# Kernel tuning notes

Measured on AMD Instinct MI355X. Metric: run time of the kernel, lower is better.

The kernel has to match this reference:

```python
import jax, jax.numpy as jnp
import numpy as np

B, T, S, C, E, H = 4, 2048, 2048, 256, 512, 8
D = E // H
SCALE = E ** (-0.5)


def setup_inputs() -> dict:
    key = jax.random.key(0)
    ks = jax.random.split(key, 12)
    x = jax.random.normal(ks[0], (B, T, C), dtype=jnp.float32)
    context = jax.random.normal(ks[1], (B, S, E), dtype=jnp.float32)
    pad_mask = jax.random.randint(ks[2], (B, T, S), 0, 2) == 1
    p = 0.02
    # Conv1d kernel_size=1 weights stored squeezed: [out_ch, in_ch]
    w_in = jax.random.normal(ks[3], (E, C), dtype=jnp.float32) * p
    b_in = jnp.zeros((E,), dtype=jnp.float32)
    wq = jax.random.normal(ks[4], (E, E), dtype=jnp.float32) * p
    bq = jnp.zeros((E,), dtype=jnp.float32)
    wk = jax.random.normal(ks[5], (E, E), dtype=jnp.float32) * p
    bk = jnp.zeros((E,), dtype=jnp.float32)
    wv = jax.random.normal(ks[6], (E, E), dtype=jnp.float32) * p
    bv = jnp.zeros((E,), dtype=jnp.float32)
    w_out = jax.random.normal(ks[7], (C, E), dtype=jnp.float32) * p
    b_out = jnp.zeros((C,), dtype=jnp.float32)
    return {"x": x, "context": context, "pad_mask": pad_mask,
            "w_in": w_in, "b_in": b_in, "wq": wq, "bq": bq,
            "wk": wk, "bk": bk, "wv": wv, "bv": bv,
            "w_out": w_out, "b_out": b_out}


def reference(x, context, pad_mask, w_in, b_in, wq, bq, wk, bk, wv, bv, w_out, b_out):
    # proj_in: Conv1d k=1 == per-token linear on channel dim. [B,T,C] -> [B,T,E]
    xe = jnp.einsum('btc,ec->bte', x, w_in) + b_in
    Q = (xe @ wq.T + bq).reshape(B, T, H, D)       # query tokens
    K = (context @ wk.T + bk).reshape(B, S, H, D)  # key tokens
    V = (context @ wv.T + bv).reshape(B, S, H, D)
    att = jnp.einsum('bihd,bjhd->bhij', Q, K) * SCALE  # [B,H,T,S]
    att = jnp.where(pad_mask[:, None, :, :], jnp.float32(-1e9), att)
    att = jax.nn.softmax(att, axis=-1)
    out = jnp.einsum('bhij,bjhd->bihd', att, V).reshape(B, T, E)
    # proj_out: Conv1d k=1, [B,T,E] -> [B,T,C]
    out = jnp.einsum('bte,ce->btc', out, w_out) + b_out
    return out
```

## Files before the change

### kernel.cpp

```cpp
#include <hip/hip_runtime.h>
#include <cstdint>
#include <cstddef>

#define Bb 4
#define Tt 2048
#define Ssz 2048
#define Cc 256
#define Ee 512
#define Hh 8

typedef short bf8 __attribute__((ext_vector_type(8)));
typedef float f4 __attribute__((ext_vector_type(4)));
typedef float f16v __attribute__((ext_vector_type(16)));
typedef unsigned int u32x2 __attribute__((ext_vector_type(2)));
typedef unsigned int u32x4 __attribute__((ext_vector_type(4)));

__device__ __forceinline__ unsigned short f2bf(float x) {
  unsigned int u = __float_as_uint(x);
  u += 0x7fffu + ((u >> 16) & 1u);
  return (unsigned short)(u >> 16);
}

__device__ __forceinline__ bf8 cvt8(float4 a, float4 b) {
  bf8 r;
  r[0] = (short)f2bf(a.x); r[1] = (short)f2bf(a.y);
  r[2] = (short)f2bf(a.z); r[3] = (short)f2bf(a.w);
  r[4] = (short)f2bf(b.x); r[5] = (short)f2bf(b.y);
  r[6] = (short)f2bf(b.z); r[7] = (short)f2bf(b.w);
  return r;
}

#if __has_builtin(__builtin_amdgcn_perm)
#define PACK2(u0, u1) __builtin_amdgcn_perm((u1), (u0), 0x07060302u)
#else
#define PACK2(u0, u1) (((u0) >> 16) | ((u1) & 0xffff0000u))
#endif

#define EXPU(v) __float_as_uint(__builtin_amdgcn_exp2f(v))
#define MFMA32(a, b, c) __builtin_amdgcn_mfma_f32_32x32x16_bf16((a), (b), (c), 0, 0, 0)

__device__ __forceinline__ void pl32swap(unsigned int& a, unsigned int& b) {
#if __has_builtin(__builtin_amdgcn_permlane32_swap)
  u32x2 r = __builtin_amdgcn_permlane32_swap(a, b, false, false);
  a = r[0];
  b = r[1];
#else
  unsigned int ax = (unsigned int)__shfl_xor((int)a, 32);
  unsigned int bx = (unsigned int)__shfl_xor((int)b, 32);
  bool hi = (threadIdx.x & 32) != 0;
  unsigned int an = hi ? bx : a;
  unsigned int bn = hi ? b : ax;
  a = an;
  b = bn;
#endif
}

__global__ __launch_bounds__(256) void prep(const float* __restrict__ w_in,
                                            const float* __restrict__ b_in,
                                            const float* __restrict__ wq,
                                            const float* __restrict__ bq,
                                            const float* __restrict__ wk,
                                            const float* __restrict__ wv,
                                            const float* __restrict__ wo,
                                            unsigned short* __restrict__ wkvb,
                                            unsigned short* __restrict__ wob,
                                            unsigned short* __restrict__ wqin,
                                            float* __restrict__ bqinb, float qsc) {
  __shared__ unsigned short sh[128][72];
  const int bid = blockIdx.x, tid = threadIdx.x;
  if (bid < 512) {
    int i = bid * 256 + tid;
    const float* s = (i < 65536) ? wk : wv;
    int off = (i < 65536) ? i : i - 65536;
    float4 v = ((const float4*)s)[off];
    ushort4 o;
    o.x = f2bf(v.x); o.y = f2bf(v.y); o.z = f2bf(v.z); o.w = f2bf(v.w);
    ((ushort4*)wkvb)[i] = o;
  } else if (bid < 640) {
    int i = (bid - 512) * 256 + tid;
    float4 v = ((const float4*)wo)[i];
    ushort4 o;
    o.x = f2bf(v.x); o.y = f2bf(v.y); o.z = f2bf(v.z); o.w = f2bf(v.w);
    ((ushort4*)wob)[i] = o;
  } else if (bid < 672) {
    const int idx = bid - 640;
    const int m0 = (idx & 7) * 64, n0 = (idx >> 3) * 64;
    unsigned short (*As)[72] = (unsigned short (*)[72]) & sh[0][0];
    unsigned short (*Bs)[72] = (unsigned short (*)[72]) & sh[64][0];
    const int wave = tid >> 6, lane = tid & 63;
    const int lrow = lane & 15, quad = lane >> 4;
    const int wm = (wave >> 1) * 32, wn = (wave & 1) * 32;
    const int arow = tid >> 3, ac = tid & 7;
    f4 acc[2][2];
#pragma unroll
    for (int i = 0; i < 2; i++)
#pragma unroll
      for (int j = 0; j < 2; j++) {
        f4 z = {0.f, 0.f, 0.f, 0.f};
        acc[i][j] = z;
      }
    for (int kt = 0; kt < 8; kt++) {
#pragma unroll
      for (int i = 0; i < 2; i++) {
        int row = arow + i * 32;
        const float* src = wq + (size_t)(m0 + row) * Ee + kt * 64 + ac * 8;
        float4 v0 = *(const float4*)src, v1 = *(const float4*)(src + 4);
        bf8 av;
        av[0] = (short)f2bf(v0.x * qsc); av[1] = (short)f2bf(v0.y * qsc);
        av[2] = (short)f2bf(v0.z * qsc); av[3] = (short)f2bf(v0.w * qsc);
        av[4] = (short)f2bf(v1.x * qsc); av[5] = (short)f2bf(v1.y * qsc);
        av[6] = (short)f2bf(v1.z * qsc); av[7] = (short)f2bf(v1.w * qsc);
        *(bf8*)&As[row][ac * 8] = av;
        int c = n0 + row;
        bf8 bv;
#pragma unroll
        for (int k = 0; k < 8; k++)
          bv[k] = (short)f2bf(w_in[(size_t)(kt * 64 + ac * 8 + k) * Cc + c]);
        *(bf8*)&Bs[row][ac * 8] = bv;
      }
      __syncthreads();
#pragma unroll
      for (int kk = 0; kk < 2; kk++) {
        bf8 af[2], bff[2];
#pragma unroll
        for (int i = 0; i < 2; i++) af[i] = *(const bf8*)&As[wm + i * 16 + lrow][kk * 32 + quad * 8];
#pragma unroll
        for (int j = 0; j < 2; j++) bff[j] = *(const bf8*)&Bs[wn + j * 16 + lrow][kk * 32 + quad * 8];
#pragma unroll
        for (int i = 0; i < 2; i++)
#pragma unroll
          for (int j = 0; j < 2; j++)
            acc[i][j] = __builtin_amdgcn_mfma_f32_16x16x32_bf16(af[i], bff[j], acc[i][j], 0, 0, 0);
      }
      __syncthreads();
    }
#pragma unroll
    for (int j = 0; j < 2; j++)
#pragma unroll
      for (int i = 0; i < 2; i++)
#pragma unroll
        for (int r = 0; r < 4; r++)
          wqin[(size_t)(m0 + wm + i * 16 + quad * 4 + r) * Cc + n0 + wn + j * 16 + lrow] =
              f2bf(acc[i][j][r]);
  } else {
    const int o = (bid - 672) * 32 + (tid >> 3);
    const int k0 = (tid & 7) * 64;
    float s = 0.f;
#pragma unroll
    for (int i = 0; i < 16; i++) {
      float4 w = *(const float4*)(wq + (size_t)o * Ee + k0 + i * 4);
      float4 bb = *(const float4*)(b_in + k0 + i * 4);
      s += w.x * bb.x + w.y * bb.y + w.z * bb.z + w.w * bb.w;
    }
    s += __shfl_xor(s, 1);
    s += __shfl_xor(s, 2);
    s += __shfl_xor(s, 4);
    if ((tid & 7) == 0) bqinb[o] = (s + bq[o]) * qsc;
  }
}

__global__ __launch_bounds__(256) void qkv(const float* __restrict__ x,
                                           const float* __restrict__ ctx,
                                           const unsigned short* __restrict__ wqin,
                                           const float* __restrict__ bqinb,
                                           const unsigned short* __restrict__ wkv,
                                           const float* __restrict__ bk,
                                           const float* __restrict__ bv,
                                           unsigned short* __restrict__ Qb,
                                           unsigned short* __restrict__ Kb,
                                           unsigned short* __restrict__ Vt,
                                           const int* __restrict__ mask,
                                           unsigned int* __restrict__ mp) {
  __shared__ unsigned short As[128][72];
  __shared__ unsigned short Bs[128][72];
  const int bid = blockIdx.x, tid = threadIdx.x;
  if (bid >= 768) {
    int i = (bid - 768) * 256 + tid;
    const int4* src = (const int4*)mask + (size_t)i * 8;
    unsigned int w = 0;
#pragma unroll
    for (int k = 0; k < 8; k++) {
      int4 v = src[k];
      w |= (unsigned int)(v.x != 0) << (k * 4);
      w |= (unsigned int)(v.y != 0) << (k * 4 + 1);
      w |= (unsigned int)(v.z != 0) << (k * 4 + 2);
      w |= (unsigned int)(v.w != 0) << (k * 4 + 3);
    }
    mp[i] = w;
    return;
  }
  const bool isQ = bid < 256;
  const int idx = isQ ? bid : bid - 256;
  const int m0 = (idx & 63) * 128;
  const int n0 = (idx >> 6) * 128;
  const int K = isQ ? 256 : 512;
  const float* A = isQ ? x : ctx;
  const unsigned short* Bt = isQ ? wqin : wkv;

  const int wave = tid >> 6, lane = tid & 63;
  const int lrow = lane & 15, quad = lane >> 4;
  const int wm = (wave >> 1) * 64, wn = (wave & 1) * 64;
  const int arow = tid >> 3, ac = tid & 7;

  f4 acc[4][4];
#pragma unroll
  for (int i = 0; i < 4; i++)
#pragma unroll
    for (int j = 0; j < 4; j++) {
      f4 z = {0.f, 0.f, 0.f, 0.f};
      acc[i][j] = z;
    }

  float4 ap0[4], ap1[4];
  bf8 bpre[4];
#pragma unroll
  for (int i = 0; i < 4; i++) {
    const float* src = A + (size_t)(m0 + arow + i * 32) * K + ac * 8;
    ap0[i] = *(const float4*)src;
    ap1[i] = *(const float4*)(src + 4);
    bpre[i] = *(const bf8*)(Bt + (size_t)(n0 + arow + i * 32) * K + ac * 8);
  }

  const int nkt = K >> 6;
  for (int kt = 0; kt < nkt; ++kt) {
#pragma unroll
    for (int i = 0; i < 4; i++) {
      *(bf8*)&As[arow + i * 32][ac * 8] = cvt8(ap0[i], ap1[i]);
      *(bf8*)&Bs[arow + i * 32][ac * 8] = bpre[i];
    }
    __syncthreads();
    if (kt + 1 < nkt) {
      int k0 = (kt + 1) << 6;
#pragma unroll
      for (int i = 0; i < 4; i++) {
        const float* src = A + (size_t)(m0 + arow + i * 32) * K + k0 + ac * 8;
        ap0[i] = *(const float4*)src;
        ap1[i] = *(const float4*)(src + 4);
        bpre[i] = *(const bf8*)(Bt + (size_t)(n0 + arow + i * 32) * K + k0 + ac * 8);
      }
    }
#pragma unroll
    for (int kk = 0; kk < 2; kk++) {
      bf8 af[4], bff[4];
#pragma unroll
      for (int i = 0; i < 4; i++)
        af[i] = *(const bf8*)&As[wm + i * 16 + lrow][kk * 32 + quad * 8];
#pragma unroll
      for (int j = 0; j < 4; j++)
        bff[j] = *(const bf8*)&Bs[wn + j * 16 + lrow][kk * 32 + quad * 8];
#pragma unroll
      for (int i = 0; i < 4; i++)
#pragma unroll
        for (int j = 0; j < 4; j++)
          acc[i][j] = __builtin_amdgcn_mfma_f32_16x16x32_bf16(af[i], bff[j],
                                                              acc[i][j], 0, 0, 0);
    }
    __syncthreads();
  }

  if (isQ) {
#pragma unroll
    for (int j = 0; j < 4; j++) {
      int col = n0 + wn + j * 16 + lrow;
      float bvv = bqinb[col];
#pragma unroll
      for (int i = 0; i < 4; i++)
#pragma unroll
        for (int r = 0; r < 4; r++)
          Qb[(size_t)(m0 + wm + i * 16 + quad * 4 + r) * Ee + col] =
              f2bf(acc[i][j][r] + bvv);
    }
  } else if (n0 < 512) {
#pragma unroll
    for (int j = 0; j < 4; j++) {
      int col = n0 + wn + j * 16 + lrow;
      float bvv = bk[col];
#pragma unroll
      for (int i = 0; i < 4; i++)
#pragma unroll
        for (int r = 0; r < 4; r++)
          Kb[(size_t)(m0 + wm + i * 16 + quad * 4 + r) * Ee + col] =
              f2bf(acc[i][j][r] + bvv);
    }
  } else {
#pragma unroll
    for (int j = 0; j < 4; j++) {
      int d = n0 - 512 + wn + j * 16 + lrow;
      int h = d >> 6, dd = d & 63;
      float bvv = bv[d];
#pragma unroll
      for (int i = 0; i < 4; i++) {
        int tok = m0 + wm + i * 16 + quad * 4;
        int b = tok >> 11, sl = tok & 2047;
        ushort4 pk;
        pk.x = f2bf(acc[i][j][0] + bvv);
        pk.y = f2bf(acc[i][j][1] + bvv);
        pk.z = f2bf(acc[i][j][2] + bvv);
        pk.w = f2bf(acc[i][j][3] + bvv);
        *(ushort4*)(Vt + (size_t)((b * Hh + h) * 64 + dd) * Ssz + sl) = pk;
      }
    }
  }
}

template <bool OUT_BF16, int BM, int BN, int WGM>
__global__ __launch_bounds__(256) void gemm_bt(const unsigned short* __restrict__ A,
                                               const unsigned short* __restrict__ Bt,
                                               const float* __restrict__ bias0,
                                               void* __restrict__ Cout,
                                               int M, int N, int K) {
  constexpr int WGN = 4 / WGM;
  constexpr int MI = BM / (WGM * 16);
  constexpr int NJ = BN / (WGN * 16);
  constexpr int NA = BM / 32;
  constexpr int NB = BN / 32;
  __shared__ unsigned short As[BM][72];
  __shared__ unsigned short Bs[BN][72];
  const int tid = threadIdx.x;
  const int wave = tid >> 6, lane = tid & 63;
  const int lrow = lane & 15, quad = lane >> 4;
  const int wm = (wave / WGN) * (BM / WGM);
  const int wn = (wave % WGN) * (BN / WGN);
  const int m0 = blockIdx.x * BM, n0 = blockIdx.y * BN;
  const int arow = tid >> 3, ac = tid & 7;

  f4 acc[MI][NJ];
#pragma unroll
  for (int i = 0; i < MI; i++)
#pragma unroll
    for (int j = 0; j < NJ; j++) {
      f4 z = {0.f, 0.f, 0.f, 0.f};
      acc[i][j] = z;
    }

  bf8 apre[NA], bpre[NB];
#pragma unroll
  for (int i = 0; i < NA; i++)
    apre[i] = *(const bf8*)(A + (size_t)(m0 + arow + i * 32) * K + ac * 8);
#pragma unroll
  for (int i = 0; i < NB; i++)
    bpre[i] = *(const bf8*)(Bt + (size_t)(n0 + arow + i * 32) * K + ac * 8);

  const int nkt = K >> 6;
  for (int kt = 0; kt < nkt; ++kt) {
#pragma unroll
    for (int i = 0; i < NA; i++) *(bf8*)&As[arow + i * 32][ac * 8] = apre[i];
#pragma unroll
    for (int i = 0; i < NB; i++) *(bf8*)&Bs[arow + i * 32][ac * 8] = bpre[i];
    __syncthreads();
    if (kt + 1 < nkt) {
      int k0 = (kt + 1) << 6;
#pragma unroll
      for (int i = 0; i < NA; i++)
        apre[i] = *(const bf8*)(A + (size_t)(m0 + arow + i * 32) * K + k0 + ac * 8);
#pragma unroll
      for (int i = 0; i < NB; i++)
        bpre[i] = *(const bf8*)(Bt + (size_t)(n0 + arow + i * 32) * K + k0 + ac * 8);
    }
#pragma unroll
    for (int kk = 0; kk < 2; kk++) {
      bf8 af[MI], bff[NJ];
#pragma unroll
      for (int i = 0; i < MI; i++)
        af[i] = *(const bf8*)&As[wm + i * 16 + lrow][kk * 32 + quad * 8];
#pragma unroll
      for (int j = 0; j < NJ; j++)
        bff[j] = *(const bf8*)&Bs[wn + j * 16 + lrow][kk * 32 + quad * 8];
#pragma unroll
      for (int i = 0; i < MI; i++)
#pragma unroll
        for (int j = 0; j < NJ; j++)
          acc[i][j] = __builtin_amdgcn_mfma_f32_16x16x32_bf16(af[i], bff[j],
                                                              acc[i][j], 0, 0, 0);
    }
    __syncthreads();
  }

#pragma unroll
  for (int j = 0; j < NJ; j++) {
    int col = n0 + wn + j * 16 + lrow;
    float bvv = bias0 ? bias0[col] : 0.f;
#pragma unroll
    for (int i = 0; i < MI; i++) {
#pragma unroll
      for (int r = 0; r < 4; r++) {
        int row = m0 + wm + i * 16 + quad * 4 + r;
        float v = acc[i][j][r] + bvv;
        if (OUT_BF16)
          ((unsigned short*)Cout)[(size_t)row * N + col] = f2bf(v);
        else
          ((float*)Cout)[(size_t)row * N + col] = v;
      }
    }
  }
}

__global__ __launch_bounds__(256, 2) void attn(const unsigned short* __restrict__ Q,
                                               const unsigned short* __restrict__ K,
                                               const unsigned short* __restrict__ Vt,
                                               const unsigned int* __restrict__ mp,
                                               unsigned short* __restrict__ O) {
  __shared__ unsigned short Ks[2][64][72];
  __shared__ unsigned short Vts[2][64][72];
  const int tid = threadIdx.x;
  const int wave = tid >> 6, lane = tid & 63;
  const int l31 = lane & 31, hi = lane >> 5;
  const int bid = blockIdx.x;
  const int bh = bid & 31, b = bh >> 3, h = bh & 7;
  const int t0 = (bid >> 5) * 128;
  const int wm = wave * 32;
  const int arow = tid >> 3, ac = tid & 7;

  const unsigned short* Qrow =
      Q + (size_t)(b * Tt + t0 + wm + l31) * Ee + h * 64 + hi * 8;
  bf8 qf[4];
#pragma unroll
  for (int c = 0; c < 4; c++) qf[c] = *(const bf8*)(Qrow + c * 16);

  f16v oacc0, oacc1, dacc;
#pragma unroll
  for (int r = 0; r < 16; r++) {
    oacc0[r] = 0.f;
    oacc1[r] = 0.f;
    dacc[r] = 0.f;
  }
  bf8 ones;
#pragma unroll
  for (int k = 0; k < 8; k++) ones[k] = (short)0x3F80;

  const unsigned short* Kbase = K + (size_t)b * Ssz * Ee + h * 64;
  const unsigned short* Vbase = Vt + (size_t)((b * Hh + h) * 64) * Ssz;
  const unsigned int* mroww = mp + (size_t)(b * Tt + t0 + wm + l31) * 64;

  bf8 kreg[2], vreg[2];
#pragma unroll
  for (int i = 0; i < 2; i++) {
    int row = arow + i * 32;
    kreg[i] = *(const bf8*)(Kbase + (size_t)row * Ee + ac * 8);
    vreg[i] = *(const bf8*)(Vbase + (size_t)row * Ssz + ac * 8);
  }
#pragma unroll
  for (int i = 0; i < 2; i++) {
    int row = arow + i * 32;
    *(bf8*)&Ks[0][row][ac * 8] = kreg[i];
    *(bf8*)&Vts[0][row][ac * 8] = vreg[i];
  }
  __syncthreads();

  for (int n = 0; n < 32; n++) {
    const int s0 = n * 64;
    const int cur = n & 1;
    if (n + 1 < 32) {
#pragma unroll
      for (int i = 0; i < 2; i++) {
        int row = arow + i * 32;
        kreg[i] = *(const bf8*)(Kbase + (size_t)(s0 + 64 + row) * Ee + ac * 8);
        vreg[i] = *(const bf8*)(Vbase + (size_t)row * Ssz + s0 + 64 + ac * 8);
      }
    }
    const uint2 mw = *(const uint2*)(mroww + (s0 >> 5));
    const unsigned int wsh0 = mw.x >> (4 * hi);
    const unsigned int wsh1 = mw.y >> (4 * hi);

    f16v sa0, sa1;
#pragma unroll
    for (int r = 0; r < 16; r++) {
      const int sh = (r & 3) + 8 * (r >> 2);
      sa0[r] = ((wsh0 >> sh) & 1u) ? -1e9f : 0.f;
      sa1[r] = ((wsh1 >> sh) & 1u) ? -1e9f : 0.f;
    }
#pragma unroll
    for (int c = 0; c < 4; c++) {
      bf8 kf0 = *(const bf8*)&Ks[cur][l31][c * 16 + hi * 8];
      bf8 kf1 = *(const bf8*)&Ks[cur][32 + l31][c * 16 + hi * 8];
      sa0 = MFMA32(kf0, qf[c], sa0);
      sa1 = MFMA32(kf1, qf[c], sa1);
    }
    unsigned int X0[8], X1[8];
#pragma unroll
    for (int m = 0; m < 8; m++) {
      X0[m] = PACK2(EXPU(sa0[2 * m]), EXPU(sa0[2 * m + 1]));
      X1[m] = PACK2(EXPU(sa1[2 * m]), EXPU(sa1[2 * m + 1]));
    }
#pragma unroll
    for (int c = 0; c < 4; c++) {
      const int m0 = 4 * (c & 1);
      unsigned int a0, a1, a2, a3;
      if (c < 2) {
        a0 = X0[m0]; a1 = X0[m0 + 1]; a2 = X0[m0 + 2]; a3 = X0[m0 + 3];
      } else {
        a0 = X1[m0]; a1 = X1[m0 + 1]; a2 = X1[m0 + 2]; a3 = X1[m0 + 3];
      }
      pl32swap(a0, a2);
      pl32swap(a1, a3);
      u32x4 pdv;
      pdv[0] = a0; pdv[1] = a1; pdv[2] = a2; pdv[3] = a3;
      bf8 pa = *(bf8*)&pdv;
      bf8 vf0 = *(const bf8*)&Vts[cur][l31][c * 16 + hi * 8];
      bf8 vf1 = *(const bf8*)&Vts[cur][32 + l31][c * 16 + hi * 8];
      dacc = MFMA32(pa, ones, dacc);
      oacc0 = MFMA32(pa, vf0, oacc0);
      oacc1 = MFMA32(pa, vf1, oacc1);
    }
    if (n + 1 < 32) {
#pragma unroll
      for (int i = 0; i < 2; i++) {
        int row = arow + i * 32;
        *(bf8*)&Ks[cur ^ 1][row][ac * 8] = kreg[i];
        *(bf8*)&Vts[cur ^ 1][row][ac * 8] = vreg[i];
      }
    }
    __syncthreads();
  }

#pragma unroll
  for (int r = 0; r < 16; r++) {
    const int tl = (r & 3) + 8 * (r >> 2) + 4 * hi;
    const float inv = 1.0f / dacc[r];
    const size_t off = (size_t)(b * Tt + t0 + wm + tl) * Ee + h * 64 + l31;
    O[off] = f2bf(oacc0[r] * inv);
    O[off + 32] = f2bf(oacc1[r] * inv);
  }
}

extern "C" void kernel_launch(void* const* d_in, const int* in_sizes, int n_in,
                              void* d_out, int out_size, void* d_ws, size_t ws_size,
                              hipStream_t stream) {
  const float* x    = (const float*)d_in[0];
  const float* ctx  = (const float*)d_in[1];
  const int*   mask = (const int*)d_in[2];
  const float* w_in = (const float*)d_in[3];
  const float* b_in = (const float*)d_in[4];
  const float* wq   = (const float*)d_in[5];
  const float* bq   = (const float*)d_in[6];
  const float* wk   = (const float*)d_in[7];
  const float* bk   = (const float*)d_in[8];
  const float* wv   = (const float*)d_in[9];
  const float* bv   = (const float*)d_in[10];
  const float* wo   = (const float*)d_in[11];
  const float* bo   = (const float*)d_in[12];

  const float qsc = 0.04419417382415922f * 1.4426950408889634f;

  unsigned short* ws = (unsigned short*)d_ws;
  unsigned int*   maskp = (unsigned int*)ws;
  unsigned short* wkvb  = ws + 1048576;
  unsigned short* wob   = ws + 1572864;
  unsigned short* wqin  = ws + 1703936;
  float*          bqinb = (float*)(ws + 1835008);
  unsigned short* Qb    = ws + 1836032;
  unsigned short* Kb    = ws + 6030336;
  unsigned short* Vtb   = ws + 10224640;
  unsigned short* Ob    = ws + 14418944;

  prep<<<688, 256, 0, stream>>>(w_in, b_in, wq, bq, wk, wv, wo,
                                wkvb, wob, wqin, bqinb, qsc);
  qkv<<<2816, 256, 0, stream>>>(x, ctx, wqin, bqinb, wkvb, bk, bv, Qb, Kb, Vtb,
                                mask, maskp);
  attn<<<512, 256, 0, stream>>>(Qb, Kb, Vtb, maskp, Ob);
  gemm_bt<false, 64, 64, 2><<<dim3(128, 4), 256, 0, stream>>>(
      Ob, wob, bo, d_out, 8192, 256, 512);
}
```

Measured before the change: 228.3 us.

## Process 64 query rows per wave in attention to reuse K/V fragments

Each attention wave now handles two 32-row query blocks instead of one, so each K and V fragment read from shared memory feeds twice as many MFMAs. The block tile grows to 256 query rows, the grid halves to 256 blocks, and launch bounds drop to one block per SM to make room for the doubled accumulators. This cuts LDS traffic and K/V global reloads per query row, but it uses more registers and leaves only 256 blocks, which may underfill a 256-CU MI355X and lower latency hiding.

```diff
diff --git a/kernel.cpp b/kernel.cpp
--- a/kernel.cpp
+++ b/kernel.cpp
@@ -395,7 +395,7 @@
   }
 }
 
-__global__ __launch_bounds__(256, 2) void attn(const unsigned short* __restrict__ Q,
+__global__ __launch_bounds__(256, 1) void attn(const unsigned short* __restrict__ Q,
                                                const unsigned short* __restrict__ K,
                                                const unsigned short* __restrict__ Vt,
                                                const unsigned int* __restrict__ mp,
@@ -407,22 +407,28 @@
   const int l31 = lane & 31, hi = lane >> 5;
   const int bid = blockIdx.x;
   const int bh = bid & 31, b = bh >> 3, h = bh & 7;
-  const int t0 = (bid >> 5) * 128;
-  const int wm = wave * 32;
+  const int t0 = (bid >> 5) * 256;
+  const int tw = t0 + wave * 64;
   const int arow = tid >> 3, ac = tid & 7;
 
-  const unsigned short* Qrow =
-      Q + (size_t)(b * Tt + t0 + wm + l31) * Ee + h * 64 + hi * 8;
-  bf8 qf[4];
-#pragma unroll
-  for (int c = 0; c < 4; c++) qf[c] = *(const bf8*)(Qrow + c * 16);
-
-  f16v oacc0, oacc1, dacc;
-#pragma unroll
-  for (int r = 0; r < 16; r++) {
-    oacc0[r] = 0.f;
-    oacc1[r] = 0.f;
-    dacc[r] = 0.f;
+  bf8 qf[2][4];
+#pragma unroll
+  for (int tb = 0; tb < 2; tb++) {
+    const unsigned short* Qrow =
+        Q + (size_t)(b * Tt + tw + tb * 32 + l31) * Ee + h * 64 + hi * 8;
+#pragma unroll
+    for (int c = 0; c < 4; c++) qf[tb][c] = *(const bf8*)(Qrow + c * 16);
+  }
+
+  f16v oacc[2][2], dacc[2];
+#pragma unroll
+  for (int tb = 0; tb < 2; tb++) {
+#pragma unroll
+    for (int r = 0; r < 16; r++) {
+      oacc[tb][0][r] = 0.f;
+      oacc[tb][1][r] = 0.f;
+      dacc[tb][r] = 0.f;
+    }
   }
   bf8 ones;
 #pragma unroll
@@ -430,7 +436,8 @@
 
   const unsigned short* Kbase = K + (size_t)b * Ssz * Ee + h * 64;
   const unsigned short* Vbase = Vt + (size_t)((b * Hh + h) * 64) * Ssz;
-  const unsigned int* mroww = mp + (size_t)(b * Tt + t0 + wm + l31) * 64;
+  const unsigned int* mrow[2] = {mp + (size_t)(b * Tt + tw + l31) * 64,
+                                 mp + (size_t)(b * Tt + tw + 32 + l31) * 64};
 
   bf8 kreg[2], vreg[2];
 #pragma unroll
@@ -458,49 +465,67 @@
         vreg[i] = *(const bf8*)(Vbase + (size_t)row * Ssz + s0 + 64 + ac * 8);
       }
     }
-    const uint2 mw = *(const uint2*)(mroww + (s0 >> 5));
-    const unsigned int wsh0 = mw.x >> (4 * hi);
-    const unsigned int wsh1 = mw.y >> (4 * hi);
-
-    f16v sa0, sa1;
-#pragma unroll
-    for (int r = 0; r < 16; r++) {
-      const int sh = (r & 3) + 8 * (r >> 2);
-      sa0[r] = ((wsh0 >> sh) & 1u) ? -1e9f : 0.f;
-      sa1[r] = ((wsh1 >> sh) & 1u) ? -1e9f : 0.f;
+    uint2 mw[2];
+#pragma unroll
+    for (int tb = 0; tb < 2; tb++) mw[tb] = *(const uint2*)(mrow[tb] + (s0 >> 5));
+
+    f16v sa0[2], sa1[2];
+#pragma unroll
+    for (int tb = 0; tb < 2; tb++) {
+      const unsigned int w0 = mw[tb].x >> (4 * hi);
+      const unsigned int w1 = mw[tb].y >> (4 * hi);
+#pragma unroll
+      for (int r = 0; r < 16; r++) {
+        const int sh = (r & 3) + 8 * (r >> 2);
+        sa0[tb][r] = ((w0 >> sh) & 1u) ? -1e9f : 0.f;
+        sa1[tb][r] = ((w1 >> sh) & 1u) ? -1e9f : 0.f;
+      }
     }
 #pragma unroll
     for (int c = 0; c < 4; c++) {
       bf8 kf0 = *(const bf8*)&Ks[cur][l31][c * 16 + hi * 8];
       bf8 kf1 = *(const bf8*)&Ks[cur][32 + l31][c * 16 + hi * 8];
-      sa0 = MFMA32(kf0, qf[c], sa0);
-      sa1 = MFMA32(kf1, qf[c], sa1);
-    }
-    unsigned int X0[8], X1[8];
-#pragma unroll
-    for (int m = 0; m < 8; m++) {
-      X0[m] = PACK2(EXPU(sa0[2 * m]), EXPU(sa0[2 * m + 1]));
-      X1[m] = PACK2(EXPU(sa1[2 * m]), EXPU(sa1[2 * m + 1]));
+#pragma unroll
+      for (int tb = 0; tb < 2; tb++) {
+        sa0[tb] = MFMA32(kf0, qf[tb][c], sa0[tb]);
+        sa1[tb] = MFMA32(kf1, qf[tb][c], sa1[tb]);
+      }
+    }
+    bf8 pa[2][4];
+#pragma unroll
+    for (int tb = 0; tb < 2; tb++) {
+      unsigned int X0[8], X1[8];
+#pragma unroll
+      for (int m = 0; m < 8; m++) {
+        X0[m] = PACK2(EXPU(sa0[tb][2 * m]), EXPU(sa0[tb][2 * m + 1]));
+        X1[m] = PACK2(EXPU(sa1[tb][2 * m]), EXPU(sa1[tb][2 * m + 1]));
+      }
+#pragma unroll
+      for (int c = 0; c < 4; c++) {
+        const int m0 = 4 * (c & 1);
+        unsigned int a0, a1, a2, a3;
+        if (c < 2) {
+          a0 = X0[m0]; a1 = X0[m0 + 1]; a2 = X0[m0 + 2]; a3 = X0[m0 + 3];
+        } else {
+          a0 = X1[m0]; a1 = X1[m0 + 1]; a2 = X1[m0 + 2]; a3 = X1[m0 + 3];
+        }
+        pl32swap(a0, a2);
+        pl32swap(a1, a3);
+        u32x4 pdv;
+        pdv[0] = a0; pdv[1] = a1; pdv[2] = a2; pdv[3] = a3;
+        pa[tb][c] = *(bf8*)&pdv;
+      }
     }
 #pragma unroll
     for (int c = 0; c < 4; c++) {
-      const int m0 = 4 * (c & 1);
-      unsigned int a0, a1, a2, a3;
-      if (c < 2) {
-        a0 = X0[m0]; a1 = X0[m0 + 1]; a2 = X0[m0 + 2]; a3 = X0[m0 + 3];
-      } else {
-        a0 = X1[m0]; a1 = X1[m0 + 1]; a2 = X1[m0 + 2]; a3 = X1[m0 + 3];
-      }
-      pl32swap(a0, a2);
-      pl32swap(a1, a3);
-      u32x4 pdv;
-      pdv[0] = a0; pdv[1] = a1; pdv[2] = a2; pdv[3] = a3;
-      bf8 pa = *(bf8*)&pdv;
       bf8 vf0 = *(const bf8*)&Vts[cur][l31][c * 16 + hi * 8];
       bf8 vf1 = *(const bf8*)&Vts[cur][32 + l31][c * 16 + hi * 8];
-      dacc = MFMA32(pa, ones, dacc);
-      oacc0 = MFMA32(pa, vf0, oacc0);
-      oacc1 = MFMA32(pa, vf1, oacc1);
+#pragma unroll
+      for (int tb = 0; tb < 2; tb++) {
+        dacc[tb] = MFMA32(pa[tb][c], ones, dacc[tb]);
+        oacc[tb][0] = MFMA32(pa[tb][c], vf0, oacc[tb][0]);
+        oacc[tb][1] = MFMA32(pa[tb][c], vf1, oacc[tb][1]);
+      }
     }
     if (n + 1 < 32) {
 #pragma unroll
@@ -514,12 +539,15 @@
   }
 
 #pragma unroll
-  for (int r = 0; r < 16; r++) {
-    const int tl = (r & 3) + 8 * (r >> 2) + 4 * hi;
-    const float inv = 1.0f / dacc[r];
-    const size_t off = (size_t)(b * Tt + t0 + wm + tl) * Ee + h * 64 + l31;
-    O[off] = f2bf(oacc0[r] * inv);
-    O[off + 32] = f2bf(oacc1[r] * inv);
+  for (int tb = 0; tb < 2; tb++) {
+#pragma unroll
+    for (int r = 0; r < 16; r++) {
+      const int tl = (r & 3) + 8 * (r >> 2) + 4 * hi;
+      const float inv = 1.0f / dacc[tb][r];
+      const size_t off = (size_t)(b * Tt + tw + tb * 32 + tl) * Ee + h * 64 + l31;
+      O[off] = f2bf(oacc[tb][0][r] * inv);
+      O[off + 32] = f2bf(oacc[tb][1][r] * inv);
+    }
   }
 }
 
@@ -557,7 +585,7 @@
                                 wkvb, wob, wqin, bqinb, qsc);
   qkv<<<2816, 256, 0, stream>>>(x, ctx, wqin, bqinb, wkvb, bk, bv, Qb, Kb, Vtb,
                                 mask, maskp);
-  attn<<<512, 256, 0, stream>>>(Qb, Kb, Vtb, maskp, Ob);
+  attn<<<256, 256, 0, stream>>>(Qb, Kb, Vtb, maskp, Ob);
   gemm_bt<false, 64, 64, 2><<<dim3(128, 4), 256, 0, stream>>>(
       Ob, wob, bo, d_out, 8192, 256, 512);
 }
```

After: 243.5 us. 1.07x slower.

## Split attention over key dimension into two halves and merge partial results

Applied to the files above, without the earlier changes.

The attention kernel now splits the key/value sequence into two halves, launching twice as many blocks, each writing unnormalized partial outputs (bf16) and row denominators. A new merge kernel sums the two partial outputs and divides by the combined denominator. This raises parallelism from 512 blocks to 1024 on a many-CU GPU, and launch bounds are raised to 4 blocks per CU. MFMA sections are also wrapped in s_setprio. It adds an extra kernel launch, extra memory traffic, and bf16 rounding of the unnormalized partial sums. Skipping the running max is safe because of the tiny weight scale.

```diff
diff --git a/kernel.cpp b/kernel.cpp
--- a/kernel.cpp
+++ b/kernel.cpp
@@ -19,6 +19,10 @@
   unsigned int u = __float_as_uint(x);
   u += 0x7fffu + ((u >> 16) & 1u);
   return (unsigned short)(u >> 16);
+}
+
+__device__ __forceinline__ float bf2f(unsigned short x) {
+  return __uint_as_float(((unsigned int)x) << 16);
 }
 
 __device__ __forceinline__ bf8 cvt8(float4 a, float4 b) {
@@ -395,11 +399,13 @@
   }
 }
 
-__global__ __launch_bounds__(256, 2) void attn(const unsigned short* __restrict__ Q,
+__global__ __launch_bounds__(256, 4) void attn(const unsigned short* __restrict__ Q,
                                                const unsigned short* __restrict__ K,
                                                const unsigned short* __restrict__ Vt,
                                                const unsigned int* __restrict__ mp,
-                                               unsigned short* __restrict__ O) {
+                                               unsigned short* __restrict__ O1,
+                                               unsigned short* __restrict__ O2,
+                                               float* __restrict__ dpart) {
   __shared__ unsigned short Ks[2][64][72];
   __shared__ unsigned short Vts[2][64][72];
   const int tid = threadIdx.x;
@@ -407,7 +413,10 @@
   const int l31 = lane & 31, hi = lane >> 5;
   const int bid = blockIdx.x;
   const int bh = bid & 31, b = bh >> 3, h = bh & 7;
-  const int t0 = (bid >> 5) * 128;
+  const int q5 = bid >> 5;
+  const int t0 = (q5 & 15) * 128;
+  const int sh = q5 >> 4;
+  const int sbase = sh << 10;
   const int wm = wave * 32;
   const int arow = tid >> 3, ac = tid & 7;
 
@@ -428,9 +437,10 @@
 #pragma unroll
   for (int k = 0; k < 8; k++) ones[k] = (short)0x3F80;
 
-  const unsigned short* Kbase = K + (size_t)b * Ssz * Ee + h * 64;
-  const unsigned short* Vbase = Vt + (size_t)((b * Hh + h) * 64) * Ssz;
-  const unsigned int* mroww = mp + (size_t)(b * Tt + t0 + wm + l31) * 64;
+  const unsigned short* Kbase = K + ((size_t)b * Ssz + sbase) * Ee + h * 64;
+  const unsigned short* Vbase = Vt + (size_t)((b * Hh + h) * 64) * Ssz + sbase;
+  const unsigned int* mroww =
+      mp + (size_t)(b * Tt + t0 + wm + l31) * 64 + (sbase >> 5);
 
   bf8 kreg[2], vreg[2];
 #pragma unroll
@@ -447,10 +457,10 @@
   }
   __syncthreads();
 
-  for (int n = 0; n < 32; n++) {
+  for (int n = 0; n < 16; n++) {
     const int s0 = n * 64;
     const int cur = n & 1;
-    if (n + 1 < 32) {
+    if (n + 1 < 16) {
 #pragma unroll
       for (int i = 0; i < 2; i++) {
         int row = arow + i * 32;
@@ -465,10 +475,11 @@
     f16v sa0, sa1;
 #pragma unroll
     for (int r = 0; r < 16; r++) {
-      const int sh = (r & 3) + 8 * (r >> 2);
-      sa0[r] = ((wsh0 >> sh) & 1u) ? -1e9f : 0.f;
-      sa1[r] = ((wsh1 >> sh) & 1u) ? -1e9f : 0.f;
-    }
+      const int shft = (r & 3) + 8 * (r >> 2);
+      sa0[r] = ((wsh0 >> shft) & 1u) ? -1e9f : 0.f;
+      sa1[r] = ((wsh1 >> shft) & 1u) ? -1e9f : 0.f;
+    }
+    __builtin_amdgcn_s_setprio(1);
 #pragma unroll
     for (int c = 0; c < 4; c++) {
       bf8 kf0 = *(const bf8*)&Ks[cur][l31][c * 16 + hi * 8];
@@ -476,12 +487,14 @@
       sa0 = MFMA32(kf0, qf[c], sa0);
       sa1 = MFMA32(kf1, qf[c], sa1);
     }
+    __builtin_amdgcn_s_setprio(0);
     unsigned int X0[8], X1[8];
 #pragma unroll
     for (int m = 0; m < 8; m++) {
       X0[m] = PACK2(EXPU(sa0[2 * m]), EXPU(sa0[2 * m + 1]));
       X1[m] = PACK2(EXPU(sa1[2 * m]), EXPU(sa1[2 * m + 1]));
     }
+    __builtin_amdgcn_s_setprio(1);
 #pragma unroll
     for (int c = 0; c < 4; c++) {
       const int m0 = 4 * (c & 1);
@@ -502,7 +515,8 @@
       oacc0 = MFMA32(pa, vf0, oacc0);
       oacc1 = MFMA32(pa, vf1, oacc1);
     }
-    if (n + 1 < 32) {
+    __builtin_amdgcn_s_setprio(0);
+    if (n + 1 < 16) {
 #pragma unroll
       for (int i = 0; i < 2; i++) {
         int row = arow + i * 32;
@@ -513,14 +527,45 @@
     __syncthreads();
   }
 
+  unsigned short* Op = sh ? O2 : O1;
+  float* dp = dpart + ((((size_t)sh * Bb + b) * Hh + h) << 11) + t0 + wm;
 #pragma unroll
   for (int r = 0; r < 16; r++) {
     const int tl = (r & 3) + 8 * (r >> 2) + 4 * hi;
-    const float inv = 1.0f / dacc[r];
     const size_t off = (size_t)(b * Tt + t0 + wm + tl) * Ee + h * 64 + l31;
-    O[off] = f2bf(oacc0[r] * inv);
-    O[off + 32] = f2bf(oacc1[r] * inv);
-  }
+    Op[off] = f2bf(oacc0[r]);
+    Op[off + 32] = f2bf(oacc1[r]);
+    if (l31 == 0) dp[tl] = dacc[r];
+  }
+}
+
+__global__ __launch_bounds__(256) void merge(unsigned short* __restrict__ O1,
+                                             const unsigned short* __restrict__ O2,
+                                             const float* __restrict__ dpart) {
+  const int i = blockIdx.x * 256 + threadIdx.x;
+  const int row = i >> 6;
+  const int c8 = i & 63;
+  const int h = c8 >> 3;
+  const int b = row >> 11, t = row & 2047;
+  const float d1 = dpart[(size_t)(b * Hh + h) * Tt + t];
+  const float d2 = dpart[(size_t)((Bb + b) * Hh + h) * Tt + t];
+  const float inv = 1.0f / (d1 + d2);
+  const size_t off = (size_t)row * Ee + c8 * 8;
+  ushort4 a0 = *(const ushort4*)(O1 + off);
+  ushort4 a1 = *(const ushort4*)(O1 + off + 4);
+  ushort4 b0 = *(const ushort4*)(O2 + off);
+  ushort4 b1 = *(const ushort4*)(O2 + off + 4);
+  ushort4 o0, o1;
+  o0.x = f2bf((bf2f(a0.x) + bf2f(b0.x)) * inv);
+  o0.y = f2bf((bf2f(a0.y) + bf2f(b0.y)) * inv);
+  o0.z = f2bf((bf2f(a0.z) + bf2f(b0.z)) * inv);
+  o0.w = f2bf((bf2f(a0.w) + bf2f(b0.w)) * inv);
+  o1.x = f2bf((bf2f(a1.x) + bf2f(b1.x)) * inv);
+  o1.y = f2bf((bf2f(a1.y) + bf2f(b1.y)) * inv);
+  o1.z = f2bf((bf2f(a1.z) + bf2f(b1.z)) * inv);
+  o1.w = f2bf((bf2f(a1.w) + bf2f(b1.w)) * inv);
+  *(ushort4*)(O1 + off) = o0;
+  *(ushort4*)(O1 + off + 4) = o1;
 }
 
 extern "C" void kernel_launch(void* const* d_in, const int* in_sizes, int n_in,
@@ -552,12 +597,15 @@
   unsigned short* Kb    = ws + 6030336;
   unsigned short* Vtb   = ws + 10224640;
   unsigned short* Ob    = ws + 14418944;
+  unsigned short* O2b   = ws + 18613248;
+  float*          dpart = (float*)(ws + 22807552);
 
   prep<<<688, 256, 0, stream>>>(w_in, b_in, wq, bq, wk, wv, wo,
                                 wkvb, wob, wqin, bqinb, qsc);
   qkv<<<2816, 256, 0, stream>>>(x, ctx, wqin, bqinb, wkvb, bk, bv, Qb, Kb, Vtb,
                                 mask, maskp);
-  attn<<<512, 256, 0, stream>>>(Qb, Kb, Vtb, maskp, Ob);
+  attn<<<1024, 256, 0, stream>>>(Qb, Kb, Vtb, maskp, Ob, O2b, dpart);
+  merge<<<2048, 256, 0, stream>>>(Ob, O2b, dpart);
   gemm_bt<false, 64, 64, 2><<<dim3(128, 4), 256, 0, stream>>>(
       Ob, wob, bo, d_out, 8192, 256, 512);
 }
```

Result: slower. 248.0 us (+8.7%).

## Store K/V in MFMA fragment order and load operands directly from global

Applied to the files above, without the earlier changes.

The qkv kernel now writes K and V in a pre-swizzled layout that matches the MFMA operand fragments, so each lane fetches its bf8 fragment with one coalesced load. The attention kernel drops the LDS double buffer and its __syncthreads, holds K fragments in registers with a one-tile-ahead prefetch, and loads V fragments straight from global memory. Wave priority is raised around the MFMA sections. This removes LDS traffic and block barriers, but every wave now reads K/V from global/L2 independently (four times per block), and the K stores in qkv become scattered 2-byte writes.

```diff
diff --git a/kernel.cpp b/kernel.cpp
--- a/kernel.cpp
+++ b/kernel.cpp
@@ -167,8 +167,8 @@
                                            const float* __restrict__ bk,
                                            const float* __restrict__ bv,
                                            unsigned short* __restrict__ Qb,
-                                           unsigned short* __restrict__ Kb,
-                                           unsigned short* __restrict__ Vt,
+                                           unsigned short* __restrict__ Kf,
+                                           unsigned short* __restrict__ Vf,
                                            const int* __restrict__ mask,
                                            unsigned int* __restrict__ mp) {
   __shared__ unsigned short As[128][72];
@@ -274,30 +274,40 @@
 #pragma unroll
     for (int j = 0; j < 4; j++) {
       int col = n0 + wn + j * 16 + lrow;
+      int h = col >> 6, dloc = col & 63;
+      int cc = dloc >> 4, hh = (dloc >> 3) & 1, ee = dloc & 7;
       float bvv = bk[col];
 #pragma unroll
       for (int i = 0; i < 4; i++)
 #pragma unroll
-        for (int r = 0; r < 4; r++)
-          Kb[(size_t)(m0 + wm + i * 16 + quad * 4 + r) * Ee + col] =
-              f2bf(acc[i][j][r] + bvv);
+        for (int r = 0; r < 4; r++) {
+          int tok = m0 + wm + i * 16 + quad * 4 + r;
+          int bb = tok >> 11, ss = tok & 2047;
+          size_t addr = (((size_t)(bb * Hh + h) * 64 + (ss >> 5)) * 4 + cc) * 512 +
+                        (hh * 32 + (ss & 31)) * 8 + ee;
+          Kf[addr] = f2bf(acc[i][j][r] + bvv);
+        }
     }
   } else {
 #pragma unroll
     for (int j = 0; j < 4; j++) {
       int d = n0 - 512 + wn + j * 16 + lrow;
       int h = d >> 6, dd = d & 63;
+      int l31 = dd & 31, dh = dd >> 5;
       float bvv = bv[d];
 #pragma unroll
       for (int i = 0; i < 4; i++) {
         int tok = m0 + wm + i * 16 + quad * 4;
-        int b = tok >> 11, sl = tok & 2047;
+        int bb = tok >> 11, sl = tok & 2047;
+        int stile = sl >> 6, cc = (sl >> 4) & 3, hh = (sl >> 3) & 1, e0 = sl & 7;
         ushort4 pk;
         pk.x = f2bf(acc[i][j][0] + bvv);
         pk.y = f2bf(acc[i][j][1] + bvv);
         pk.z = f2bf(acc[i][j][2] + bvv);
         pk.w = f2bf(acc[i][j][3] + bvv);
-        *(ushort4*)(Vt + (size_t)((b * Hh + h) * 64 + dd) * Ssz + sl) = pk;
+        size_t addr = ((((size_t)(bb * Hh + h) * 32 + stile) * 4 + cc) * 2 + dh) * 512 +
+                      (hh * 32 + l31) * 8 + e0;
+        *(ushort4*)(Vf + addr) = pk;
       }
     }
   }
@@ -396,12 +406,10 @@
 }
 
 __global__ __launch_bounds__(256, 2) void attn(const unsigned short* __restrict__ Q,
-                                               const unsigned short* __restrict__ K,
-                                               const unsigned short* __restrict__ Vt,
+                                               const unsigned short* __restrict__ Kf,
+                                               const unsigned short* __restrict__ Vf,
                                                const unsigned int* __restrict__ mp,
                                                unsigned short* __restrict__ O) {
-  __shared__ unsigned short Ks[2][64][72];
-  __shared__ unsigned short Vts[2][64][72];
   const int tid = threadIdx.x;
   const int wave = tid >> 6, lane = tid & 63;
   const int l31 = lane & 31, hi = lane >> 5;
@@ -409,7 +417,6 @@
   const int bh = bid & 31, b = bh >> 3, h = bh & 7;
   const int t0 = (bid >> 5) * 128;
   const int wm = wave * 32;
-  const int arow = tid >> 3, ac = tid & 7;
 
   const unsigned short* Qrow =
       Q + (size_t)(b * Tt + t0 + wm + l31) * Ee + h * 64 + hi * 8;
@@ -428,36 +435,27 @@
 #pragma unroll
   for (int k = 0; k < 8; k++) ones[k] = (short)0x3F80;
 
-  const unsigned short* Kbase = K + (size_t)b * Ssz * Ee + h * 64;
-  const unsigned short* Vbase = Vt + (size_t)((b * Hh + h) * 64) * Ssz;
+  const unsigned short* Kl = Kf + (size_t)bh * 131072 + lane * 8;
+  const unsigned short* Vl = Vf + (size_t)bh * 131072 + lane * 8;
   const unsigned int* mroww = mp + (size_t)(b * Tt + t0 + wm + l31) * 64;
 
-  bf8 kreg[2], vreg[2];
-#pragma unroll
-  for (int i = 0; i < 2; i++) {
-    int row = arow + i * 32;
-    kreg[i] = *(const bf8*)(Kbase + (size_t)row * Ee + ac * 8);
-    vreg[i] = *(const bf8*)(Vbase + (size_t)row * Ssz + ac * 8);
-  }
-#pragma unroll
-  for (int i = 0; i < 2; i++) {
-    int row = arow + i * 32;
-    *(bf8*)&Ks[0][row][ac * 8] = kreg[i];
-    *(bf8*)&Vts[0][row][ac * 8] = vreg[i];
-  }
-  __syncthreads();
-
-  for (int n = 0; n < 32; n++) {
-    const int s0 = n * 64;
-    const int cur = n & 1;
-    if (n + 1 < 32) {
-#pragma unroll
-      for (int i = 0; i < 2; i++) {
-        int row = arow + i * 32;
-        kreg[i] = *(const bf8*)(Kbase + (size_t)(s0 + 64 + row) * Ee + ac * 8);
-        vreg[i] = *(const bf8*)(Vbase + (size_t)row * Ssz + s0 + 64 + ac * 8);
-      }
-    }
+  bf8 ka[2][4], kb[2][4];
+
+  auto pfk = [&](bf8 (&KD)[2][4], int s0) {
+#pragma unroll
+    for (int sb = 0; sb < 2; sb++)
+#pragma unroll
+      for (int c = 0; c < 4; c++)
+        KD[sb][c] = *(const bf8*)(Kl + (((((s0 >> 5) + sb) * 4) + c) << 9));
+  };
+
+  auto body = [&](bf8 (&KF)[2][4], bf8 (&KN)[2][4], int s0, bool dopf) {
+    bf8 vf[4][2];
+#pragma unroll
+    for (int c = 0; c < 4; c++)
+#pragma unroll
+      for (int dh = 0; dh < 2; dh++)
+        vf[c][dh] = *(const bf8*)(Vl + (((((s0 >> 6) * 4 + c) * 2) + dh) << 9));
     const uint2 mw = *(const uint2*)(mroww + (s0 >> 5));
     const unsigned int wsh0 = mw.x >> (4 * hi);
     const unsigned int wsh1 = mw.y >> (4 * hi);
@@ -465,23 +463,25 @@
     f16v sa0, sa1;
 #pragma unroll
     for (int r = 0; r < 16; r++) {
-      const int sh = (r & 3) + 8 * (r >> 2);
-      sa0[r] = ((wsh0 >> sh) & 1u) ? -1e9f : 0.f;
-      sa1[r] = ((wsh1 >> sh) & 1u) ? -1e9f : 0.f;
-    }
+      const int shft = (r & 3) + 8 * (r >> 2);
+      sa0[r] = ((wsh0 >> shft) & 1u) ? -1e9f : 0.f;
+      sa1[r] = ((wsh1 >> shft) & 1u) ? -1e9f : 0.f;
+    }
+    __builtin_amdgcn_s_setprio(1);
 #pragma unroll
     for (int c = 0; c < 4; c++) {
-      bf8 kf0 = *(const bf8*)&Ks[cur][l31][c * 16 + hi * 8];
-      bf8 kf1 = *(const bf8*)&Ks[cur][32 + l31][c * 16 + hi * 8];
-      sa0 = MFMA32(kf0, qf[c], sa0);
-      sa1 = MFMA32(kf1, qf[c], sa1);
-    }
+      sa0 = MFMA32(KF[0][c], qf[c], sa0);
+      sa1 = MFMA32(KF[1][c], qf[c], sa1);
+    }
+    __builtin_amdgcn_s_setprio(0);
+    if (dopf) pfk(KN, s0 + 64);
     unsigned int X0[8], X1[8];
 #pragma unroll
     for (int m = 0; m < 8; m++) {
       X0[m] = PACK2(EXPU(sa0[2 * m]), EXPU(sa0[2 * m + 1]));
       X1[m] = PACK2(EXPU(sa1[2 * m]), EXPU(sa1[2 * m + 1]));
     }
+    __builtin_amdgcn_s_setprio(1);
 #pragma unroll
     for (int c = 0; c < 4; c++) {
       const int m0 = 4 * (c & 1);
@@ -496,21 +496,17 @@
       u32x4 pdv;
       pdv[0] = a0; pdv[1] = a1; pdv[2] = a2; pdv[3] = a3;
       bf8 pa = *(bf8*)&pdv;
-      bf8 vf0 = *(const bf8*)&Vts[cur][l31][c * 16 + hi * 8];
-      bf8 vf1 = *(const bf8*)&Vts[cur][32 + l31][c * 16 + hi * 8];
       dacc = MFMA32(pa, ones, dacc);
-      oacc0 = MFMA32(pa, vf0, oacc0);
-      oacc1 = MFMA32(pa, vf1, oacc1);
-    }
-    if (n + 1 < 32) {
-#pragma unroll
-      for (int i = 0; i < 2; i++) {
-        int row = arow + i * 32;
-        *(bf8*)&Ks[cur ^ 1][row][ac * 8] = kreg[i];
-        *(bf8*)&Vts[cur ^ 1][row][ac * 8] = vreg[i];
-      }
-    }
-    __syncthreads();
+      oacc0 = MFMA32(pa, vf[c][0], oacc0);
+      oacc1 = MFMA32(pa, vf[c][1], oacc1);
+    }
+    __builtin_amdgcn_s_setprio(0);
+  };
+
+  pfk(ka, 0);
+  for (int s0 = 0; s0 < Ssz; s0 += 128) {
+    body(ka, kb, s0, true);
+    body(kb, ka, s0 + 64, s0 + 128 < Ssz);
   }
 
 #pragma unroll
@@ -549,15 +545,15 @@
   unsigned short* wqin  = ws + 1703936;
   float*          bqinb = (float*)(ws + 1835008);
   unsigned short* Qb    = ws + 1836032;
-  unsigned short* Kb    = ws + 6030336;
-  unsigned short* Vtb   = ws + 10224640;
+  unsigned short* Kfb   = ws + 6030336;
+  unsigned short* Vfb   = ws + 10224640;
   unsigned short* Ob    = ws + 14418944;
 
   prep<<<688, 256, 0, stream>>>(w_in, b_in, wq, bq, wk, wv, wo,
                                 wkvb, wob, wqin, bqinb, qsc);
-  qkv<<<2816, 256, 0, stream>>>(x, ctx, wqin, bqinb, wkvb, bk, bv, Qb, Kb, Vtb,
+  qkv<<<2816, 256, 0, stream>>>(x, ctx, wqin, bqinb, wkvb, bk, bv, Qb, Kfb, Vfb,
                                 mask, maskp);
-  attn<<<512, 256, 0, stream>>>(Qb, Kb, Vtb, maskp, Ob);
+  attn<<<512, 256, 0, stream>>>(Qb, Kfb, Vfb, maskp, Ob);
   gemm_bt<false, 64, 64, 2><<<dim3(128, 4), 256, 0, stream>>>(
       Ob, wob, bo, d_out, 8192, 256, 512);
 }
```

Measured after the change: 230.4 us. Within noise of the previous version (+0.9%).
